# Performance work log

Measured on AMD Instinct MI355X. Metric: run time of the kernel, lower is better.

The kernel has to match this reference:

```python
import jax, jax.numpy as jnp
import numpy as np

TAU = 1.0
LAM = 1.0


def _l2_normalize(x, axis=-1, eps=1e-12):
    n = jnp.sqrt(jnp.sum(x * x, axis=axis, keepdims=True))
    return x / jnp.maximum(n, eps)


def setup_inputs() -> dict:
    key = jax.random.key(0)
    k1, k2, k3, k4 = jax.random.split(key, 4)
    B, D = 4096, 512
    return {
        "mu": jax.random.normal(k1, (B, D), dtype=jnp.float32),
        "mu_cap": jax.random.normal(k2, (B, D), dtype=jnp.float32),
        "log_var": jax.random.normal(k3, (B, D), dtype=jnp.float32),
        "log_var_cap": jax.random.normal(k4, (B, D), dtype=jnp.float32),
    }


def _supcon(features, labels, tau):
    # features: [N, D], labels: [N]
    N = features.shape[0]
    Xn = _l2_normalize(features, axis=-1)
    sim = Xn @ Xn.T                                   # [N, N] cosine similarities
    eye = jnp.eye(N, dtype=bool)
    sim = jnp.where(eye, -jnp.inf, sim)               # fill_diagonal_(-inf)
    ls = jax.nn.log_softmax(sim / tau, axis=-1)
    ls = jnp.where(eye, 0.0, ls)                      # fill_diagonal_(0)
    mask = (labels[:, None] == labels[None, :]).astype(jnp.float32)
    mask = jnp.where(eye, 0.0, mask)
    num_pos = jnp.sum(mask, axis=-1)
    pos_avg = jnp.sum(ls * mask, axis=-1) / (num_pos + 1e-5)
    return -jnp.sum(pos_avg) / N


def _kl_div(mu1, mu2, logvar1, logvar2):
    var1 = jnp.exp(logvar1)
    var2 = jnp.exp(logvar2)
    part1 = (var1 + 1e-8) / (var2 + 1e-8)
    part2 = logvar2 - logvar1
    part3 = jnp.square(mu1 - mu2) / (var2 + 1e-8)
    return 0.5 * jnp.sum(part1 + part2 + part3 - 1.0, axis=1)


def reference(mu, mu_cap, log_var, log_var_cap):
    B, D = mu.shape
    # reparameterization (fixed noise for a deterministic reference)
    ek1, ek2 = jax.random.split(jax.random.key(42))
    eps1 = jax.random.normal(ek1, (B, D), dtype=mu.dtype)
    eps2 = jax.random.normal(ek2, (B, D), dtype=mu.dtype)
    x = mu + jnp.exp(0.5 * log_var) * eps1
    x_cap = mu_cap + jnp.exp(0.5 * log_var_cap) * eps2

    # SimCLR: concat views, fake labels [0..B-1, 0..B-1]
    feats = jnp.concatenate([x, x_cap], axis=0)       # [2B, D]
    labels = jnp.concatenate([jnp.arange(B), jnp.arange(B)])
    base_loss = _supcon(feats, labels, TAU)

    # distribution alignment (JSD between Gaussians), on L2-normalized stats
    mu_n = _l2_normalize(mu, axis=1)
    lv_n = _l2_normalize(log_var, axis=1)
    mu_cn = _l2_normalize(mu_cap, axis=1)
    lv_cn = _l2_normalize(log_var_cap, axis=1)
    mu_m = 0.5 * (mu_n + mu_cn)
    log_var_m = jnp.log(0.5 * (jnp.exp(lv_n) + jnp.exp(lv_cn)) + 1e-8)
    kl1 = _kl_div(mu_n, mu_m, lv_n, log_var_m)
    kl2 = _kl_div(mu_cn, mu_m, lv_cn, log_var_m)
    jsd = jnp.mean(0.5 * (kl1 + kl2))

    return base_loss + LAM * jsd
```

## Files before the change

kernel.cpp:

```cpp
#include <hip/hip_runtime.h>
#include <hip/hip_bf16.h>
#include <stdint.h>


typedef __attribute__((ext_vector_type(4))) float f32x4;
typedef __attribute__((ext_vector_type(8))) short bf16x8;

#define NSLOT 32
#define NGK   16

__device__ __forceinline__ uint32_t fmix32(uint32_t h){
  h ^= h >> 16; h *= 0x85ebca6bu;
  h ^= h >> 13; h *= 0xc2b2ae35u;
  h ^= h >> 16; return h;
}

__device__ __forceinline__ void bm_pair(uint32_t b1, uint32_t b2,
                                        float& z0, float& z1){
  float u1 = (float)((b1 >> 9) + 1u) * 1.1920929e-7f;
  float u2 = (float)(b2 >> 9)        * 1.1920929e-7f;
  float r  = sqrtf(-2.0f * __logf(u1));
  float th = 6.2831853f * u2;
  z0 = r * __cosf(th);
  z1 = r * __sinf(th);
}

__device__ __forceinline__ unsigned short f2bf(float f){
  uint32_t u = __float_as_uint(f);
  u += 0x7FFFu + ((u >> 16) & 1u);
  return (unsigned short)(u >> 16);
}

__global__ __launch_bounds__(256) void k_featsjsd(const float* __restrict__ mu,
                                                  const float* __restrict__ mu_cap,
                                                  const float* __restrict__ lv,
                                                  const float* __restrict__ lv_cap,
                                                  unsigned short* __restrict__ Xn,
                                                  float* __restrict__ jsd_row){
  int t = threadIdx.x;
  int w = t >> 6, l = t & 63;
  int r = blockIdx.x * 4 + w;
  size_t base = (size_t)r * 512;
  int c0 = l * 4;

  float m[8], mc[8], av[8], bv[8];
  #pragma unroll
  for (int h = 0; h < 2; ++h){
    int c = c0 + h*256;
    float4 m4  = *(const float4*)(mu     + base + c);
    float4 mc4 = *(const float4*)(mu_cap + base + c);
    float4 av4 = *(const float4*)(lv     + base + c);
    float4 bv4 = *(const float4*)(lv_cap + base + c);
    m[h*4+0]=m4.x;  m[h*4+1]=m4.y;  m[h*4+2]=m4.z;  m[h*4+3]=m4.w;
    mc[h*4+0]=mc4.x; mc[h*4+1]=mc4.y; mc[h*4+2]=mc4.z; mc[h*4+3]=mc4.w;
    av[h*4+0]=av4.x; av[h*4+1]=av4.y; av[h*4+2]=av4.z; av[h*4+3]=av4.w;
    bv[h*4+0]=bv4.x; bv[h*4+1]=bv4.y; bv[h*4+2]=bv4.z; bv[h*4+3]=bv4.w;
  }

  float e1[8], e2[8];
  #pragma unroll
  for (int h = 0; h < 2; ++h){
    uint32_t idx0 = (uint32_t)r*512u + (uint32_t)(c0 + h*256);
    bm_pair(fmix32(idx0*0x9E3779B9u + 0xA511E9B3u),
            fmix32((idx0+1u)*0x9E3779B9u + 0xA511E9B3u), e1[h*4+0], e1[h*4+1]);
    bm_pair(fmix32((idx0+2u)*0x9E3779B9u + 0xA511E9B3u),
            fmix32((idx0+3u)*0x9E3779B9u + 0xA511E9B3u), e1[h*4+2], e1[h*4+3]);
    bm_pair(fmix32(idx0*0x9E3779B9u + 0x63D83595u),
            fmix32((idx0+1u)*0x9E3779B9u + 0x63D83595u), e2[h*4+0], e2[h*4+1]);
    bm_pair(fmix32((idx0+2u)*0x9E3779B9u + 0x63D83595u),
            fmix32((idx0+3u)*0x9E3779B9u + 0x63D83595u), e2[h*4+2], e2[h*4+3]);
  }

  float x[8], xc[8];
  float sx=0.f, sxc=0.f, sm=0.f, smc=0.f, sa=0.f, sb=0.f;
  #pragma unroll
  for (int q = 0; q < 8; ++q){
    sm  += m[q]*m[q];   smc += mc[q]*mc[q];
    sa  += av[q]*av[q]; sb  += bv[q]*bv[q];
    x[q]  = m[q]  + __expf(0.5f*av[q]) * e1[q];  sx  += x[q]*x[q];
    xc[q] = mc[q] + __expf(0.5f*bv[q]) * e2[q];  sxc += xc[q]*xc[q];
  }

  #pragma unroll
  for (int o = 1; o < 64; o <<= 1){
    sx  += __shfl_xor(sx,  o);  sxc += __shfl_xor(sxc, o);
    sm  += __shfl_xor(sm,  o);  smc += __shfl_xor(smc, o);
    sa  += __shfl_xor(sa,  o);  sb  += __shfl_xor(sb,  o);
  }
  float ix  = 1.f / fmaxf(sqrtf(sx),  1e-12f);
  float ixc = 1.f / fmaxf(sqrtf(sxc), 1e-12f);
  float im  = 1.f / fmaxf(sqrtf(sm),  1e-12f);
  float imc = 1.f / fmaxf(sqrtf(smc), 1e-12f);
  float ia  = 1.f / fmaxf(sqrtf(sa),  1e-12f);
  float ib  = 1.f / fmaxf(sqrtf(sb),  1e-12f);

  float accv = 0.f;
  #pragma unroll
  for (int h = 0; h < 2; ++h){
    unsigned short xb[4], xcb[4];
    #pragma unroll
    for (int k = 0; k < 4; ++k){
      int q = h*4 + k;
      xb[k]  = f2bf(x[q]  * ix);
      xcb[k] = f2bf(xc[q] * ixc);
      float an = m[q]*im, bn = mc[q]*imc;
      float al = av[q]*ia, bl = bv[q]*ib;
      float ea = __expf(al), eb = __expf(bl);
      float varm = 0.5f*(ea + eb);
      float vp8  = varm + 1e-8f;
      float lvm  = __logf(vp8);
      float den  = vp8 + 1e-8f;
      float dm   = 0.5f*(an - bn);
      float dm2  = dm*dm;
      accv += (ea + 1e-8f)/den + (lvm - al) + dm2/den - 1.f;
      accv += (eb + 1e-8f)/den + (lvm - bl) + dm2/den - 1.f;
    }
    int c = c0 + h*256;
    *(uint64_t*)&Xn[base + c] =
        (uint64_t)xb[0] | ((uint64_t)xb[1] << 16) |
        ((uint64_t)xb[2] << 32) | ((uint64_t)xb[3] << 48);
    *(uint64_t*)&Xn[(size_t)(4096+r)*512 + c] =
        (uint64_t)xcb[0] | ((uint64_t)xcb[1] << 16) |
        ((uint64_t)xcb[2] << 32) | ((uint64_t)xcb[3] << 48);
  }

  #pragma unroll
  for (int o = 1; o < 64; o <<= 1) accv += __shfl_xor(accv, o);
  if (l == 0) jsd_row[r] = 0.25f * accv;
}

__device__ __forceinline__ void gload_lds16(const unsigned short* g, unsigned short* l){
  __builtin_amdgcn_global_load_lds(
      (const __attribute__((address_space(1))) void*)g,
      (__attribute__((address_space(3))) void*)l, 16, 0, 0);
}

__device__ __forceinline__ void stage_slot(const unsigned short* __restrict__ Xn,
                                           unsigned short* S, int slot, int pbase,
                                           int gk, int wid, int prow, int pcol){
  const unsigned short* g = Xn + (size_t)(pbase + wid*32 + prow)*512 + gk*32 + pcol;
  gload_lds16(g,          &S[slot*8192 + (wid*2  )*512]);
  gload_lds16(g + 16*512, &S[slot*8192 + (wid*2+1)*512]);
}

__device__ __forceinline__ void gk_body(
    int gk, const unsigned short* __restrict__ Xn,
    unsigned short* SA, unsigned short* SB,
    int rowbase, int colbase, int wid, int prow, int pcol,
    int aoff, int boff,
    bf16x8 (&af0c)[4], bf16x8 (&bfc)[4],
    bf16x8 (&af0n)[4], bf16x8 (&bfn)[4],
    bf16x8 (&af1)[4],
    f32x4 (&acc)[8][4])
{
  const unsigned short* SAb = &SA[(gk & 3)*8192];

  #pragma unroll
  for (int mi = 0; mi < 4; ++mi)
    af1[mi] = *(const bf16x8*)&SAb[aoff + 2048 + mi*512];
  if (gk + 3 < NGK)
    stage_slot(Xn, SA, (gk+3)&3, rowbase, gk+3, wid, prow, pcol);
  asm volatile("s_waitcnt lgkmcnt(4)" ::: "memory");
  __builtin_amdgcn_sched_barrier(0);
  __builtin_amdgcn_s_setprio(1);
  #pragma unroll
  for (int mi = 0; mi < 4; ++mi)
    #pragma unroll
    for (int n = 0; n < 4; ++n)
      acc[mi][n] = __builtin_amdgcn_mfma_f32_16x16x32_bf16(af0c[mi], bfc[n], acc[mi][n], 0, 0, 0);
  __builtin_amdgcn_s_setprio(0);
  if (gk <= 12)      asm volatile("s_waitcnt vmcnt(6)" ::: "memory");
  else if (gk == 13) asm volatile("s_waitcnt vmcnt(4)" ::: "memory");
  else if (gk == 14) asm volatile("s_waitcnt vmcnt(0)" ::: "memory");
  __builtin_amdgcn_s_barrier();

  if (gk + 1 < NGK){
    const unsigned short* SAn = &SA[((gk+1) & 3)*8192];
    const unsigned short* SBn = &SB[((gk+1) & 3)*8192];
    #pragma unroll
    for (int n = 0; n < 4; ++n)
      bfn[n] = *(const bf16x8*)&SBn[boff + n*512];
    #pragma unroll
    for (int mi = 0; mi < 4; ++mi)
      af0n[mi] = *(const bf16x8*)&SAn[aoff + mi*512];
  }
  if (gk + 3 < NGK)
    stage_slot(Xn, SB, (gk+3)&3, colbase, gk+3, wid, prow, pcol);
  if (gk + 1 < NGK) asm volatile("s_waitcnt lgkmcnt(8)" ::: "memory");
  else              asm volatile("s_waitcnt lgkmcnt(0)" ::: "memory");
  __builtin_amdgcn_sched_barrier(0);
  __builtin_amdgcn_s_setprio(1);
  #pragma unroll
  for (int mi = 0; mi < 4; ++mi)
    #pragma unroll
    for (int n = 0; n < 4; ++n)
      acc[4+mi][n] = __builtin_amdgcn_mfma_f32_16x16x32_bf16(af1[mi], bfc[n], acc[4+mi][n], 0, 0, 0);
  __builtin_amdgcn_s_setprio(0);
  __builtin_amdgcn_s_barrier();
}

__global__ __launch_bounds__(512, 1) void k_simlse(const unsigned short* __restrict__ Xn,
                                                   float* __restrict__ rowsumP,
                                                   float* __restrict__ possim){
  int bid = (blockIdx.x & 7)*64 + (blockIdx.x >> 3);

  __shared__ unsigned short SA[4*8192];
  __shared__ unsigned short SB[4*8192];
  __shared__ float redR[4][256];
  __shared__ float redC[2][256];

  int tid = threadIdx.x;
  int wid = tid >> 6, l = tid & 63;
  int wr = wid >> 2, wn = wid & 3;
  int l15 = l & 15, l4 = l >> 4;

  int prow = (l >> 3)*2 + (((l & 7) ^ (l >> 3)) >> 2);
  int pcol = (((l & 7) ^ (l >> 3)) & 3) * 8;

  const int idx8 = (((l15 & 1) << 2) | l4) ^ (l15 >> 1);
  const int aoff = wr*4096 + (l15 >> 1)*64 + idx8*8;
  const int boff = wn*2048 + (l15 >> 1)*64 + idx8*8;

  int ntile, rb0, cb0, rb1, cb1;
  if (bid < 16){
    ntile = 2;
    rb0 = cb0 = 2*bid;
    rb1 = cb1 = 2*bid + 1;
  } else {
    ntile = 1;
    int j = bid - 16, rbb = 0, rem = 31;
    while (j >= rem){ j -= rem; --rem; ++rbb; }
    rb0 = rbb; cb0 = rbb + 1 + j;
    rb1 = cb1 = 0;
  }

  bf16x8 af0a[4], af0b[4], bfa[4], bfb[4], af1[4];

  for (int tile = 0; tile < ntile; ++tile){
    int rb = tile ? rb1 : rb0;
    int cb = tile ? cb1 : cb0;
    int rowbase = rb*256, colbase = cb*256;
    bool diag    = (rb == cb);
    bool postile = (cb == rb + 16);

    f32x4 acc[8][4];
    #pragma unroll
    for (int m = 0; m < 8; ++m)
      #pragma unroll
      for (int n = 0; n < 4; ++n) acc[m][n] = f32x4{0.f,0.f,0.f,0.f};

    if (tile) __syncthreads();

    #pragma unroll
    for (int g0 = 0; g0 < 3; ++g0){
      stage_slot(Xn, SA, g0, rowbase, g0, wid, prow, pcol);
      stage_slot(Xn, SB, g0, colbase, g0, wid, prow, pcol);
    }
    asm volatile("s_waitcnt vmcnt(8)" ::: "memory");
    __builtin_amdgcn_s_barrier();

    #pragma unroll
    for (int n = 0; n < 4; ++n)
      bfa[n] = *(const bf16x8*)&SB[boff + n*512];
    #pragma unroll
    for (int mi = 0; mi < 4; ++mi)
      af0a[mi] = *(const bf16x8*)&SA[aoff + mi*512];

    #pragma unroll
    for (int gk = 0; gk < NGK; gk += 2){
      gk_body(gk,   Xn, SA, SB, rowbase, colbase, wid, prow, pcol, aoff, boff,
              af0a, bfa, af0b, bfb, af1, acc);
      gk_body(gk+1, Xn, SA, SB, rowbase, colbase, wid, prow, pcol, aoff, boff,
              af0b, bfb, af0a, bfa, af1, acc);
    }

    #pragma unroll
    for (int m = 0; m < 8; ++m){
      #pragma unroll
      for (int n = 0; n < 4; ++n){
        int col_l = wn*64 + n*16 + l15;
        #pragma unroll
        for (int r = 0; r < 4; ++r){
          int row_l = wr*128 + m*16 + l4*4 + r;
          float v = acc[m][n][r];
          if (postile && row_l == col_l){
            possim[rowbase + row_l] = v;
            possim[colbase + col_l] = v;
          }
          float e = __expf(v);
          if (diag && row_l == col_l) e = 0.f;
          acc[m][n][r] = e;
        }
      }
    }

    #pragma unroll
    for (int m = 0; m < 8; ++m){
      #pragma unroll
      for (int r = 0; r < 4; ++r){
        float s = acc[m][0][r] + acc[m][1][r] + acc[m][2][r] + acc[m][3][r];
        s += __shfl_xor(s, 1); s += __shfl_xor(s, 2);
        s += __shfl_xor(s, 4); s += __shfl_xor(s, 8);
        if (l15 == 0) redR[wn][wr*128 + m*16 + l4*4 + r] = s;
      }
    }
    #pragma unroll
    for (int n = 0; n < 4; ++n){
      float s = 0.f;
      #pragma unroll
      for (int m = 0; m < 8; ++m)
        #pragma unroll
        for (int r = 0; r < 4; ++r) s += acc[m][n][r];
      s += __shfl_xor(s, 16); s += __shfl_xor(s, 32);
      if (l4 == 0) redC[wr][wn*64 + n*16 + l15] = s;
    }
    __syncthreads();
    if (tid < 256){
      float rs = redR[0][tid] + redR[1][tid] + redR[2][tid] + redR[3][tid];
      rowsumP[(size_t)cb*8192 + rowbase + tid] = rs;
      if (!diag){
        float cs = redC[0][tid] + redC[1][tid];
        rowsumP[(size_t)rb*8192 + colbase + tid] = cs;
      }
    }
  }
}

__global__ __launch_bounds__(256) void k_lsepart(const float* __restrict__ rowsumP,
                                                 const float* __restrict__ possim,
                                                 float* __restrict__ part){
  int t = threadIdx.x;
  int row = blockIdx.x*64 + (t & 63);
  int g = t >> 6;
  float s = 0.f;
  #pragma unroll
  for (int cs = 0; cs < 8; ++cs)
    s += rowsumP[(size_t)(g*8 + cs)*8192 + row];
  __shared__ float partial[4][64];
  partial[g][t & 63] = s;
  __syncthreads();
  if (t < 64){
    float tot = partial[0][t] + partial[1][t] + partial[2][t] + partial[3][t];
    float v = __logf(tot) - possim[row];
    #pragma unroll
    for (int o = 32; o; o >>= 1) v += __shfl_down(v, o);
    if (t == 0) part[blockIdx.x] = v;
  }
}

__global__ __launch_bounds__(256) void k_final(const float* __restrict__ part,
                                               const float* __restrict__ jsd_row,
                                               float* __restrict__ out){
  int t = threadIdx.x;
  float s = (t < 128) ? part[t] : 0.f;
  float j = 0.f;
  #pragma unroll
  for (int q = 0; q < 16; ++q) j += jsd_row[t + q*256];

  __shared__ float sr[4], jr[4];
  float ss = s, jj = j;
  #pragma unroll
  for (int o = 32; o; o >>= 1){ ss += __shfl_down(ss, o); jj += __shfl_down(jj, o); }
  if ((t & 63) == 0){ sr[t >> 6] = ss; jr[t >> 6] = jj; }
  __syncthreads();
  if (t == 0){
    float base = (sr[0]+sr[1]+sr[2]+sr[3]) / (8192.f * (1.f + 1e-5f));
    float jsd  = (jr[0]+jr[1]+jr[2]+jr[3]) / 4096.f;
    out[0] = base + jsd;
  }
}

extern "C" void kernel_launch(void* const* d_in, const int* in_sizes, int n_in,
                              void* d_out, int out_size, void* d_ws, size_t ws_size,
                              hipStream_t stream) {
  const float* mu     = (const float*)d_in[0];
  const float* mu_cap = (const float*)d_in[1];
  const float* lv     = (const float*)d_in[2];
  const float* lv_cap = (const float*)d_in[3];
  float* out = (float*)d_out;

  char* w = (char*)d_ws;
  unsigned short* Xn = (unsigned short*)w;
  float* rowsumP = (float*)(w + 8388608);
  float* possim  = (float*)(w + 8388608 + 1048576);
  float* jsd_row = (float*)(w + 8388608 + 1048576 + 32768);
  float* part    = (float*)(w + 8388608 + 1048576 + 32768 + 16384);

  k_featsjsd<<<1024, 256, 0, stream>>>(mu, mu_cap, lv, lv_cap, Xn, jsd_row);
  k_simlse  <<<512,  512, 0, stream>>>(Xn, rowsumP, possim);
  k_lsepart <<<128,  256, 0, stream>>>(rowsumP, possim, part);
  k_final   <<<1,    256, 0, stream>>>(part, jsd_row, out);
}
```

Measured before the change: 86.46 us.

## Replace 4-slot deep-prefetch GEMM pipeline with 2-stage double buffer at K=64

Replaces the GEMM main loop of the similarity kernel. The old loop prefetched three K-slices ahead, held register double buffers and used partial vmcnt/lgkmcnt waits. The new loop processes 64-wide K chunks in two halves, each loading a full set of 8 A fragments and 4 B fragments, with one double-buffered LDS stage. It simplifies the schedule and halves the number of barriers. In exchange it gives up prefetch depth, waits fully on LDS reads before each MFMA burst, and drains all global loads every iteration, so memory latency may be exposed.

New measurement: 82.66 us. -4.4%, faster.

```diff
diff --git a/kernel.cpp b/kernel.cpp
--- a/kernel.cpp
+++ b/kernel.cpp
@@ -7,7 +7,7 @@
 typedef __attribute__((ext_vector_type(8))) short bf16x8;
 
 #define NSLOT 32
-#define NGK   16
+#define NGK2  8
 
 __device__ __forceinline__ uint32_t fmix32(uint32_t h){
   h ^= h >> 16; h *= 0x85ebca6bu;
@@ -135,68 +135,12 @@
       (__attribute__((address_space(3))) void*)l, 16, 0, 0);
 }
 
-__device__ __forceinline__ void stage_slot(const unsigned short* __restrict__ Xn,
-                                           unsigned short* S, int slot, int pbase,
-                                           int gk, int wid, int prow, int pcol){
-  const unsigned short* g = Xn + (size_t)(pbase + wid*32 + prow)*512 + gk*32 + pcol;
-  gload_lds16(g,          &S[slot*8192 + (wid*2  )*512]);
-  gload_lds16(g + 16*512, &S[slot*8192 + (wid*2+1)*512]);
-}
-
-__device__ __forceinline__ void gk_body(
-    int gk, const unsigned short* __restrict__ Xn,
-    unsigned short* SA, unsigned short* SB,
-    int rowbase, int colbase, int wid, int prow, int pcol,
-    int aoff, int boff,
-    bf16x8 (&af0c)[4], bf16x8 (&bfc)[4],
-    bf16x8 (&af0n)[4], bf16x8 (&bfn)[4],
-    bf16x8 (&af1)[4],
-    f32x4 (&acc)[8][4])
-{
-  const unsigned short* SAb = &SA[(gk & 3)*8192];
-
-  #pragma unroll
-  for (int mi = 0; mi < 4; ++mi)
-    af1[mi] = *(const bf16x8*)&SAb[aoff + 2048 + mi*512];
-  if (gk + 3 < NGK)
-    stage_slot(Xn, SA, (gk+3)&3, rowbase, gk+3, wid, prow, pcol);
-  asm volatile("s_waitcnt lgkmcnt(4)" ::: "memory");
-  __builtin_amdgcn_sched_barrier(0);
-  __builtin_amdgcn_s_setprio(1);
-  #pragma unroll
-  for (int mi = 0; mi < 4; ++mi)
-    #pragma unroll
-    for (int n = 0; n < 4; ++n)
-      acc[mi][n] = __builtin_amdgcn_mfma_f32_16x16x32_bf16(af0c[mi], bfc[n], acc[mi][n], 0, 0, 0);
-  __builtin_amdgcn_s_setprio(0);
-  if (gk <= 12)      asm volatile("s_waitcnt vmcnt(6)" ::: "memory");
-  else if (gk == 13) asm volatile("s_waitcnt vmcnt(4)" ::: "memory");
-  else if (gk == 14) asm volatile("s_waitcnt vmcnt(0)" ::: "memory");
-  __builtin_amdgcn_s_barrier();
-
-  if (gk + 1 < NGK){
-    const unsigned short* SAn = &SA[((gk+1) & 3)*8192];
-    const unsigned short* SBn = &SB[((gk+1) & 3)*8192];
-    #pragma unroll
-    for (int n = 0; n < 4; ++n)
-      bfn[n] = *(const bf16x8*)&SBn[boff + n*512];
-    #pragma unroll
-    for (int mi = 0; mi < 4; ++mi)
-      af0n[mi] = *(const bf16x8*)&SAn[aoff + mi*512];
-  }
-  if (gk + 3 < NGK)
-    stage_slot(Xn, SB, (gk+3)&3, colbase, gk+3, wid, prow, pcol);
-  if (gk + 1 < NGK) asm volatile("s_waitcnt lgkmcnt(8)" ::: "memory");
-  else              asm volatile("s_waitcnt lgkmcnt(0)" ::: "memory");
-  __builtin_amdgcn_sched_barrier(0);
-  __builtin_amdgcn_s_setprio(1);
-  #pragma unroll
-  for (int mi = 0; mi < 4; ++mi)
-    #pragma unroll
-    for (int n = 0; n < 4; ++n)
-      acc[4+mi][n] = __builtin_amdgcn_mfma_f32_16x16x32_bf16(af1[mi], bfc[n], acc[4+mi][n], 0, 0, 0);
-  __builtin_amdgcn_s_setprio(0);
-  __builtin_amdgcn_s_barrier();
+__device__ __forceinline__ void stage_sub(const unsigned short* __restrict__ Xn,
+                                          unsigned short* S, int s, int pbase,
+                                          int kc, int wid, int prow, int pcol){
+  const unsigned short* g = Xn + (size_t)(pbase + wid*32 + prow)*512 + kc*32 + pcol;
+  gload_lds16(g,          &S[s*8192 + (wid*2  )*512]);
+  gload_lds16(g + 16*512, &S[s*8192 + (wid*2+1)*512]);
 }
 
 __global__ __launch_bounds__(512, 1) void k_simlse(const unsigned short* __restrict__ Xn,
@@ -234,8 +178,6 @@
     rb1 = cb1 = 0;
   }
 
-  bf16x8 af0a[4], af0b[4], bfa[4], bfb[4], af1[4];
-
   for (int tile = 0; tile < ntile; ++tile){
     int rb = tile ? rb1 : rb0;
     int cb = tile ? cb1 : cb0;
@@ -251,27 +193,68 @@
 
     if (tile) __syncthreads();
 
-    #pragma unroll
-    for (int g0 = 0; g0 < 3; ++g0){
-      stage_slot(Xn, SA, g0, rowbase, g0, wid, prow, pcol);
-      stage_slot(Xn, SB, g0, colbase, g0, wid, prow, pcol);
-    }
-    asm volatile("s_waitcnt vmcnt(8)" ::: "memory");
+    stage_sub(Xn, SA, 0, rowbase, 0, wid, prow, pcol);
+    stage_sub(Xn, SA, 1, rowbase, 1, wid, prow, pcol);
+    stage_sub(Xn, SB, 0, colbase, 0, wid, prow, pcol);
+    stage_sub(Xn, SB, 1, colbase, 1, wid, prow, pcol);
+    asm volatile("s_waitcnt vmcnt(0)" ::: "memory");
     __builtin_amdgcn_s_barrier();
 
     #pragma unroll
-    for (int n = 0; n < 4; ++n)
-      bfa[n] = *(const bf16x8*)&SB[boff + n*512];
-    #pragma unroll
-    for (int mi = 0; mi < 4; ++mi)
-      af0a[mi] = *(const bf16x8*)&SA[aoff + mi*512];
-
-    #pragma unroll
-    for (int gk = 0; gk < NGK; gk += 2){
-      gk_body(gk,   Xn, SA, SB, rowbase, colbase, wid, prow, pcol, aoff, boff,
-              af0a, bfa, af0b, bfb, af1, acc);
-      gk_body(gk+1, Xn, SA, SB, rowbase, colbase, wid, prow, pcol, aoff, boff,
-              af0b, bfb, af0a, bfa, af1, acc);
+    for (int gk = 0; gk < NGK2; ++gk){
+      int sl = gk & 1;
+      const unsigned short* S0a = &SA[(2*sl  )*8192];
+      const unsigned short* S1a = &SA[(2*sl+1)*8192];
+      const unsigned short* S0b = &SB[(2*sl  )*8192];
+      const unsigned short* S1b = &SB[(2*sl+1)*8192];
+      int ns = (gk + 1) & 1;
+
+      bf16x8 af[8], bfr[4];
+
+      #pragma unroll
+      for (int n = 0; n < 4; ++n)
+        bfr[n] = *(const bf16x8*)&S0b[boff + n*512];
+      #pragma unroll
+      for (int mi = 0; mi < 8; ++mi)
+        af[mi] = *(const bf16x8*)&S0a[aoff + mi*512];
+      if (gk + 1 < NGK2){
+        stage_sub(Xn, SA, 2*ns,   rowbase, 2*(gk+1),   wid, prow, pcol);
+        stage_sub(Xn, SA, 2*ns+1, rowbase, 2*(gk+1)+1, wid, prow, pcol);
+      }
+      asm volatile("s_waitcnt lgkmcnt(0)" ::: "memory");
+      __builtin_amdgcn_sched_barrier(0);
+      __builtin_amdgcn_s_setprio(1);
+      #pragma unroll
+      for (int mi = 0; mi < 8; ++mi)
+        #pragma unroll
+        for (int n = 0; n < 4; ++n)
+          acc[mi][n] = __builtin_amdgcn_mfma_f32_16x16x32_bf16(af[mi], bfr[n], acc[mi][n], 0, 0, 0);
+      __builtin_amdgcn_s_setprio(0);
+
+      #pragma unroll
+      for (int n = 0; n < 4; ++n)
+        bfr[n] = *(const bf16x8*)&S1b[boff + n*512];
+      #pragma unroll
+      for (int mi = 0; mi < 8; ++mi)
+        af[mi] = *(const bf16x8*)&S1a[aoff + mi*512];
+      if (gk + 1 < NGK2){
+        stage_sub(Xn, SB, 2*ns,   colbase, 2*(gk+1),   wid, prow, pcol);
+        stage_sub(Xn, SB, 2*ns+1, colbase, 2*(gk+1)+1, wid, prow, pcol);
+      }
+      asm volatile("s_waitcnt lgkmcnt(0)" ::: "memory");
+      __builtin_amdgcn_sched_barrier(0);
+      __builtin_amdgcn_s_setprio(1);
+      #pragma unroll
+      for (int mi = 0; mi < 8; ++mi)
+        #pragma unroll
+        for (int n = 0; n < 4; ++n)
+          acc[mi][n] = __builtin_amdgcn_mfma_f32_16x16x32_bf16(af[mi], bfr[n], acc[mi][n], 0, 0, 0);
+      __builtin_amdgcn_s_setprio(0);
+
+      if (gk + 1 < NGK2){
+        asm volatile("s_waitcnt vmcnt(0)" ::: "memory");
+        __builtin_amdgcn_s_barrier();
+      }
     }
 
     #pragma unroll
```
